# Performance work log

Measured on AMD Instinct MI355X. Metric: run time of the kernel, lower is better.

Reference implementation:

```python
import jax, jax.numpy as jnp
import numpy as np

B, L, S = 8192, 1024, 3
OUTSIDE, TM_HELIX, INSIDE = 0, 1, 2


def setup_inputs() -> dict:
    key = jax.random.key(0)
    k1, k2 = jax.random.split(key)
    emissions = jax.random.normal(k1, (B, L, S), dtype=jnp.float32)
    tags = jax.random.randint(k2, (B, L), 0, S)
    mask = jnp.ones((B, L), dtype=jnp.float32)
    t = np.zeros((S, S), dtype=np.float32)
    t[OUTSIDE, INSIDE] = -5.0
    t[INSIDE, OUTSIDE] = -5.0
    t[OUTSIDE, TM_HELIX] = 1.0
    t[INSIDE, TM_HELIX] = 1.0
    t[TM_HELIX, OUTSIDE] = 1.0
    t[TM_HELIX, INSIDE] = 1.0
    transitions = jnp.asarray(t)
    return {"emissions": emissions, "mask": mask, "transitions": transitions, "tags": tags}


def _score_sentence(emissions, tags, mask, transitions):
    # emission score of the gold tag at every position: (B, L)
    em_score = jnp.take_along_axis(emissions, tags[..., None], axis=2)[..., 0]
    # transition score between consecutive gold tags: (B, L-1)
    trans_score = transitions[tags[:, :-1], tags[:, 1:]]
    return em_score[:, 0] * mask[:, 0] + jnp.sum(
        (trans_score + em_score[:, 1:]) * mask[:, 1:], axis=1
    )


def _forward_alg(emissions, mask, transitions):
    def step(alpha, xs):
        em_t, m_t = xs  # (B, S), (B,)
        # scores[b, i, j] = alpha[b, i] + T[i, j] + em_t[b, j]
        scores = alpha[:, :, None] + transitions[None, :, :] + em_t[:, None, :]
        new_alpha = jax.nn.logsumexp(scores, axis=1)
        alpha = jnp.where(m_t[:, None] > 0, new_alpha, alpha)
        return alpha, None

    alpha0 = emissions[:, 0, :]
    xs = (jnp.swapaxes(emissions[:, 1:, :], 0, 1),  # (L-1, B, S)
          jnp.swapaxes(mask[:, 1:], 0, 1))          # (L-1, B)
    alpha, _ = jax.lax.scan(step, alpha0, xs)
    return jax.nn.logsumexp(alpha, axis=1)  # (B,)


def reference(emissions, mask, transitions, tags):
    logZ = _forward_alg(emissions, mask, transitions)
    gold = _score_sentence(emissions, tags, mask, transitions)
    return jnp.mean(logZ - gold)
```

## Files before the change

kernel.cpp:

```cpp
#include <hip/hip_runtime.h>


#define LOG2E 1.4426950408889634f
#define LN2   0.6931471805599453f

constexpr int B = 8192;
constexpr int L = 1024;
constexpr int SEQS_PER_BLOCK = 4;

__device__ __forceinline__ float fexp2(float x) { return __builtin_amdgcn_exp2f(x); }
__device__ __forceinline__ float flog2(float x) { return __builtin_amdgcn_logf(x); }

__device__ __forceinline__ float f4get(const float4& v, int c) {
  return c == 0 ? v.x : (c == 1 ? v.y : (c == 2 ? v.z : v.w));
}
__device__ __forceinline__ int i4get(const int4& v, int c) {
  return c == 0 ? v.x : (c == 1 ? v.y : (c == 2 ? v.z : v.w));
}

__device__ __forceinline__ float mux3(float x0, float x1, float x2, int i) {
  return (i == 0) ? x0 : ((i == 1) ? x1 : x2);
}
__device__ __forceinline__ float trmux(const float* __restrict__ T2, int p, int c) {
  const float r0 = mux3(T2[0], T2[1], T2[2], c);
  const float r1 = mux3(T2[3], T2[4], T2[5], c);
  const float r2 = mux3(T2[6], T2[7], T2[8], c);
  return mux3(r0, r1, r2, p);
}

__device__ __forceinline__ void matmul3(float* __restrict__ D,
                                        const float* __restrict__ A,
                                        const float* __restrict__ Bm) {
  #pragma unroll
  for (int i = 0; i < 3; ++i)
    #pragma unroll
    for (int j = 0; j < 3; ++j)
      D[i * 3 + j] = A[i * 3 + 0] * Bm[0 * 3 + j] +
                     A[i * 3 + 1] * Bm[1 * 3 + j] +
                     A[i * 3 + 2] * Bm[2 * 3 + j];
}

__device__ __forceinline__ void renorm3(float* __restrict__ P, float& scale) {
  float m = P[0];
  #pragma unroll
  for (int e = 1; e < 9; ++e) m = fmaxf(m, P[e]);
  int ex;
  (void)frexpf(m, &ex);
  #pragma unroll
  for (int e = 0; e < 9; ++e) P[e] = ldexpf(P[e], -ex);
  scale += (float)ex;
}

__global__ __launch_bounds__(256, 4) void crf_main(
    const float* __restrict__ em, const float* __restrict__ mask,
    const float* __restrict__ trans, const int* __restrict__ tags,
    float* __restrict__ out) {
  const int lane = threadIdx.x & 63;
  const int wid = threadIdx.x >> 6;
  const int b = blockIdx.x * SEQS_PER_BLOCK + wid;

  const float4* em4 = (const float4*)(em + (size_t)b * (L * 3)) + lane * 12;
  const float4* mk4 = (const float4*)(mask + (size_t)b * L) + lane * 4;
  const int4*   tg4 = (const int4*)(tags + (size_t)b * L) + lane * 4;

  float4 E[12];
  #pragma unroll
  for (int u = 0; u < 12; ++u) E[u] = em4[u];
  float4 MK[4];
  #pragma unroll
  for (int u = 0; u < 4; ++u) MK[u] = mk4[u];
  int4 TG[4];
  #pragma unroll
  for (int u = 0; u < 4; ++u) TG[u] = tg4[u];

  float T2[9], tk[9];
  #pragma unroll
  for (int e = 0; e < 9; ++e) {
    T2[e] = trans[e] * LOG2E;
    tk[e] = fexp2(T2[e]);
  }

  float P[9] = {1.f, 0.f, 0.f, 0.f, 1.f, 0.f, 0.f, 0.f, 1.f};
  float scale = 0.f, gold = 0.f;
  float a0 = 0.f, a1 = 0.f, a2 = 0.f;
  float e0_sel = 0.f, mk0 = 0.f;
  int tag0 = 0, prev = 0;

  #pragma unroll
  for (int s = 0; s < 16; ++s) {
    const float ev0 = f4get(E[(3 * s + 0) >> 2], (3 * s + 0) & 3) * LOG2E;
    const float ev1 = f4get(E[(3 * s + 1) >> 2], (3 * s + 1) & 3) * LOG2E;
    const float ev2 = f4get(E[(3 * s + 2) >> 2], (3 * s + 2) & 3) * LOG2E;
    const float m   = f4get(MK[s >> 2], s & 3);
    const int   cur = i4get(TG[s >> 2], s & 3);

    const float e = mux3(ev0, ev1, ev2, cur);
    if (s == 0) {
      e0_sel = e; mk0 = m; tag0 = cur;
    } else {
      gold = fmaf(trmux(T2, prev, cur) + e, m, gold);
    }
    prev = cur;

    const float w0 = fexp2(ev0);
    const float w1 = fexp2(ev1);
    const float w2 = fexp2(ev2);
    if (s == 0) { a0 = w0; a1 = w1; a2 = w2; }
    const bool act = (m > 0.f) && !(s == 0 && lane == 0);
    const float g  = act ? 1.f : 0.f;
    const float c1 = 1.f - g;
    const float u0 = w0 * g, u1 = w1 * g, u2 = w2 * g;
    float M[9];
    M[0] = fmaf(tk[0], u0, c1); M[1] = tk[1] * u1;           M[2] = tk[2] * u2;
    M[3] = tk[3] * u0;          M[4] = fmaf(tk[4], u1, c1);  M[5] = tk[5] * u2;
    M[6] = tk[6] * u0;          M[7] = tk[7] * u1;           M[8] = fmaf(tk[8], u2, c1);
    float N[9];
    matmul3(N, P, M);
    #pragma unroll
    for (int e2 = 0; e2 < 9; ++e2) P[e2] = N[e2];

    if (s == 7 || s == 15) renorm3(P, scale);
  }

  const int prevLast = __shfl_up(prev, 1);
  if (lane == 0) gold = fmaf(e0_sel, mk0, gold);
  else           gold = fmaf(trmux(T2, prevLast, tag0) + e0_sel, mk0, gold);
  #pragma unroll
  for (int d = 1; d < 64; d <<= 1) gold += __shfl_xor(gold, d, 64);

  #pragma unroll
  for (int d = 1; d < 64; d <<= 1) {
    float o[9];
    #pragma unroll
    for (int e = 0; e < 9; ++e) o[e] = __shfl_xor(P[e], d, 64);
    const float osc = __shfl_xor(scale, d, 64);
    const bool later = (lane & d) != 0;
    float A[9], Bm[9];
    #pragma unroll
    for (int e = 0; e < 9; ++e) {
      A[e]  = later ? o[e] : P[e];
      Bm[e] = later ? P[e] : o[e];
    }
    float N[9];
    matmul3(N, A, Bm);
    #pragma unroll
    for (int e = 0; e < 9; ++e) P[e] = N[e];
    scale += osc;
  }

  __shared__ float red[SEQS_PER_BLOCK];
  if (lane == 0) {
    const float z = a0 * (P[0] + P[1] + P[2]) +
                    a1 * (P[3] + P[4] + P[5]) +
                    a2 * (P[6] + P[7] + P[8]);
    red[wid] = LN2 * (scale + flog2(z) - gold);
  }
  __syncthreads();
  if (threadIdx.x == 0) {
    const float s = red[0] + red[1] + red[2] + red[3];
    atomicAdd(out, s * (1.0f / (float)B));
  }
}

extern "C" void kernel_launch(void* const* d_in, const int* in_sizes, int n_in,
                              void* d_out, int out_size, void* d_ws, size_t ws_size,
                              hipStream_t stream) {
  const float* em    = (const float*)d_in[0];
  const float* mask  = (const float*)d_in[1];
  const float* trans = (const float*)d_in[2];
  const int*   tags  = (const int*)d_in[3];
  float* out = (float*)d_out;

  hipMemsetAsync(out, 0, sizeof(float), stream);
  crf_main<<<B / SEQS_PER_BLOCK, 256, 0, stream>>>(em, mask, trans, tags, out);
}
```

Before: 196.3 us.

## Stage sequence halves through padded LDS with coalesced loads and prefetch

Global loads change from per-lane strided float4 chunks to fully coalesced wave-wide float4 loads. The data is transposed through padded shared memory so each lane still handles a contiguous segment of 8 steps. Each sequence is split into two halves of 512 steps: the second half is prefetched into registers while the first is computed, then the two 3x3 products are combined. This adds LDS traffic, an extra wave scan, and block-wide syncs, in exchange for better DRAM coalescing and overlap of loads with compute.

```diff
diff --git a/kernel.cpp b/kernel.cpp
--- a/kernel.cpp
+++ b/kernel.cpp
@@ -5,21 +5,16 @@
 #define LN2   0.6931471805599453f
 
 constexpr int B = 8192;
-constexpr int L = 1024;
-constexpr int SEQS_PER_BLOCK = 4;
+constexpr int W = 4;
+constexpr int EM_DW = 64 * 25;
+constexpr int MK_DW = 64 * 9;
+constexpr int TG_DW = 128;
 
 __device__ __forceinline__ float fexp2(float x) { return __builtin_amdgcn_exp2f(x); }
 __device__ __forceinline__ float flog2(float x) { return __builtin_amdgcn_logf(x); }
 
-__device__ __forceinline__ float f4get(const float4& v, int c) {
-  return c == 0 ? v.x : (c == 1 ? v.y : (c == 2 ? v.z : v.w));
-}
-__device__ __forceinline__ int i4get(const int4& v, int c) {
-  return c == 0 ? v.x : (c == 1 ? v.y : (c == 2 ? v.z : v.w));
-}
-
-__device__ __forceinline__ float mux3(float x0, float x1, float x2, int i) {
-  return (i == 0) ? x0 : ((i == 1) ? x1 : x2);
+__device__ __forceinline__ float mux3(float a, float b, float c, int i) {
+  return i == 0 ? a : (i == 1 ? b : c);
 }
 __device__ __forceinline__ float trmux(const float* __restrict__ T2, int p, int c) {
   const float r0 = mux3(T2[0], T2[1], T2[2], c);
@@ -51,82 +46,94 @@
   scale += (float)ex;
 }
 
-__global__ __launch_bounds__(256, 4) void crf_main(
-    const float* __restrict__ em, const float* __restrict__ mask,
-    const float* __restrict__ trans, const int* __restrict__ tags,
-    float* __restrict__ out) {
-  const int lane = threadIdx.x & 63;
-  const int wid = threadIdx.x >> 6;
-  const int b = blockIdx.x * SEQS_PER_BLOCK + wid;
-
-  const float4* em4 = (const float4*)(em + (size_t)b * (L * 3)) + lane * 12;
-  const float4* mk4 = (const float4*)(mask + (size_t)b * L) + lane * 4;
-  const int4*   tg4 = (const int4*)(tags + (size_t)b * L) + lane * 4;
-
-  float4 E[12];
-  #pragma unroll
-  for (int u = 0; u < 12; ++u) E[u] = em4[u];
-  float4 MK[4];
-  #pragma unroll
-  for (int u = 0; u < 4; ++u) MK[u] = mk4[u];
-  int4 TG[4];
-  #pragma unroll
-  for (int u = 0; u < 4; ++u) TG[u] = tg4[u];
-
-  float T2[9], tk[9];
-  #pragma unroll
-  for (int e = 0; e < 9; ++e) {
-    T2[e] = trans[e] * LOG2E;
-    tk[e] = fexp2(T2[e]);
-  }
-
-  float P[9] = {1.f, 0.f, 0.f, 0.f, 1.f, 0.f, 0.f, 0.f, 1.f};
-  float scale = 0.f, gold = 0.f;
-  float a0 = 0.f, a1 = 0.f, a2 = 0.f;
-  float e0_sel = 0.f, mk0 = 0.f;
+__device__ __forceinline__ void stage(float* __restrict__ E, float* __restrict__ Mk,
+                                      unsigned* __restrict__ Tg, int lane,
+                                      const float4* __restrict__ vem,
+                                      const float4* __restrict__ vmk,
+                                      const int4* __restrict__ vtg) {
+  #pragma unroll
+  for (int u = 0; u < 6; ++u) {
+    const int p = u * 64 + lane;
+    const int a = 4 * p + (int)((unsigned)p / 6u);
+    const float4 v = vem[u];
+    E[a + 0] = v.x; E[a + 1] = v.y; E[a + 2] = v.z; E[a + 3] = v.w;
+  }
+  #pragma unroll
+  for (int u = 0; u < 2; ++u) {
+    const int p = u * 64 + lane;
+    const int a = 4 * p + (p >> 1);
+    const float4 v = vmk[u];
+    Mk[a + 0] = v.x; Mk[a + 1] = v.y; Mk[a + 2] = v.z; Mk[a + 3] = v.w;
+  }
+  #pragma unroll
+  for (int u = 0; u < 2; ++u) {
+    const int p = u * 64 + lane;
+    const int4 t = vtg[u];
+    Tg[p] = (unsigned)(t.x & 3) | ((unsigned)(t.y & 3) << 8) |
+            ((unsigned)(t.z & 3) << 16) | ((unsigned)(t.w & 3) << 24);
+  }
+}
+
+template <bool FIRST>
+__device__ __forceinline__ void compute_round(
+    const float* __restrict__ E, const float* __restrict__ Mk,
+    const unsigned* __restrict__ Tg, int lane,
+    const float* __restrict__ T2, const float* __restrict__ tk,
+    float* __restrict__ Pout, float& scaleOut,
+    float& gold, int& lastTag, int boundaryTag, float* __restrict__ a012) {
+  const float* eml = E + 25 * lane;
+  const float* mkl = Mk + 9 * lane;
+  const unsigned t0 = Tg[2 * lane + 0];
+  const unsigned t1 = Tg[2 * lane + 1];
+
+  float P[9];
+  float scale = 0.f;
+  float e0sel = 0.f, mk0 = 0.f;
   int tag0 = 0, prev = 0;
 
   #pragma unroll
-  for (int s = 0; s < 16; ++s) {
-    const float ev0 = f4get(E[(3 * s + 0) >> 2], (3 * s + 0) & 3) * LOG2E;
-    const float ev1 = f4get(E[(3 * s + 1) >> 2], (3 * s + 1) & 3) * LOG2E;
-    const float ev2 = f4get(E[(3 * s + 2) >> 2], (3 * s + 2) & 3) * LOG2E;
-    const float m   = f4get(MK[s >> 2], s & 3);
-    const int   cur = i4get(TG[s >> 2], s & 3);
+  for (int j = 0; j < 8; ++j) {
+    const float ev0 = eml[3 * j + 0] * LOG2E;
+    const float ev1 = eml[3 * j + 1] * LOG2E;
+    const float ev2 = eml[3 * j + 2] * LOG2E;
+    const float m = mkl[j];
+    const unsigned tw = (j < 4) ? t0 : t1;
+    const int cur = (int)((tw >> (8 * (j & 3))) & 3u);
 
     const float e = mux3(ev0, ev1, ev2, cur);
-    if (s == 0) {
-      e0_sel = e; mk0 = m; tag0 = cur;
-    } else {
-      gold = fmaf(trmux(T2, prev, cur) + e, m, gold);
-    }
+    if (j == 0) { e0sel = e; mk0 = m; tag0 = cur; }
+    else        gold = fmaf(trmux(T2, prev, cur) + e, m, gold);
     prev = cur;
 
     const float w0 = fexp2(ev0);
     const float w1 = fexp2(ev1);
     const float w2 = fexp2(ev2);
-    if (s == 0) { a0 = w0; a1 = w1; a2 = w2; }
-    const bool act = (m > 0.f) && !(s == 0 && lane == 0);
-    const float g  = act ? 1.f : 0.f;
+    if (FIRST && j == 0) { a012[0] = w0; a012[1] = w1; a012[2] = w2; }
+    const bool act = (m > 0.f) && !(FIRST && j == 0 && lane == 0);
+    const float g = act ? 1.f : 0.f;
     const float c1 = 1.f - g;
     const float u0 = w0 * g, u1 = w1 * g, u2 = w2 * g;
     float M[9];
-    M[0] = fmaf(tk[0], u0, c1); M[1] = tk[1] * u1;           M[2] = tk[2] * u2;
-    M[3] = tk[3] * u0;          M[4] = fmaf(tk[4], u1, c1);  M[5] = tk[5] * u2;
-    M[6] = tk[6] * u0;          M[7] = tk[7] * u1;           M[8] = fmaf(tk[8], u2, c1);
-    float N[9];
-    matmul3(N, P, M);
-    #pragma unroll
-    for (int e2 = 0; e2 < 9; ++e2) P[e2] = N[e2];
-
-    if (s == 7 || s == 15) renorm3(P, scale);
-  }
-
-  const int prevLast = __shfl_up(prev, 1);
-  if (lane == 0) gold = fmaf(e0_sel, mk0, gold);
-  else           gold = fmaf(trmux(T2, prevLast, tag0) + e0_sel, mk0, gold);
-  #pragma unroll
-  for (int d = 1; d < 64; d <<= 1) gold += __shfl_xor(gold, d, 64);
+    M[0] = fmaf(tk[0], u0, c1); M[1] = tk[1] * u1;          M[2] = tk[2] * u2;
+    M[3] = tk[3] * u0;          M[4] = fmaf(tk[4], u1, c1); M[5] = tk[5] * u2;
+    M[6] = tk[6] * u0;          M[7] = tk[7] * u1;          M[8] = fmaf(tk[8], u2, c1);
+    if (j == 0) {
+      #pragma unroll
+      for (int e2 = 0; e2 < 9; ++e2) P[e2] = M[e2];
+    } else {
+      float N[9];
+      matmul3(N, P, M);
+      #pragma unroll
+      for (int e2 = 0; e2 < 9; ++e2) P[e2] = N[e2];
+    }
+  }
+  renorm3(P, scale);
+
+  const int prevLast = __shfl_up(prev, 1, 64);
+  const int bt = (lane == 0) ? boundaryTag : prevLast;
+  if (FIRST && lane == 0) gold = fmaf(e0sel, mk0, gold);
+  else                    gold = fmaf(trmux(T2, bt, tag0) + e0sel, mk0, gold);
+  lastTag = prev;
 
   #pragma unroll
   for (int d = 1; d < 64; d <<= 1) {
@@ -147,13 +154,80 @@
     for (int e = 0; e < 9; ++e) P[e] = N[e];
     scale += osc;
   }
-
-  __shared__ float red[SEQS_PER_BLOCK];
+  #pragma unroll
+  for (int e = 0; e < 9; ++e) Pout[e] = P[e];
+  scaleOut = scale;
+}
+
+__global__ __launch_bounds__(256, 4) void crf_main(
+    const float* __restrict__ em, const float* __restrict__ mask,
+    const float* __restrict__ trans, const int* __restrict__ tags,
+    float* __restrict__ out) {
+  __shared__ float s_em[W][EM_DW];
+  __shared__ float s_mk[W][MK_DW];
+  __shared__ unsigned s_tg[W][TG_DW];
+  __shared__ float red[W];
+
+  const int lane = threadIdx.x & 63;
+  const int wid = threadIdx.x >> 6;
+  const int b = blockIdx.x * W + wid;
+
+  const float4* em4 = (const float4*)(em + (size_t)b * 3072);
+  const float4* mk4 = (const float4*)(mask + (size_t)b * 1024);
+  const int4*   tg4 = (const int4*)(tags + (size_t)b * 1024);
+
+  float4 aem[6], amk[2]; int4 atg[2];
+  #pragma unroll
+  for (int u = 0; u < 6; ++u) aem[u] = em4[u * 64 + lane];
+  #pragma unroll
+  for (int u = 0; u < 2; ++u) amk[u] = mk4[u * 64 + lane];
+  #pragma unroll
+  for (int u = 0; u < 2; ++u) atg[u] = tg4[u * 64 + lane];
+
+  float T2[9], tk[9];
+  #pragma unroll
+  for (int e = 0; e < 9; ++e) {
+    T2[e] = trans[e] * LOG2E;
+    tk[e] = fexp2(T2[e]);
+  }
+
+  stage(s_em[wid], s_mk[wid], s_tg[wid], lane, aem, amk, atg);
+  __syncthreads();
+
+  float4 pem[6], pmk[2]; int4 ptg[2];
+  #pragma unroll
+  for (int u = 0; u < 6; ++u) pem[u] = em4[384 + u * 64 + lane];
+  #pragma unroll
+  for (int u = 0; u < 2; ++u) pmk[u] = mk4[128 + u * 64 + lane];
+  #pragma unroll
+  for (int u = 0; u < 2; ++u) ptg[u] = tg4[128 + u * 64 + lane];
+
+  float gold = 0.f;
+  float a012[3];
+  float PA[9], PB[9];
+  float scA, scB;
+  int lastA, lastB;
+
+  compute_round<true>(s_em[wid], s_mk[wid], s_tg[wid], lane, T2, tk,
+                      PA, scA, gold, lastA, 0, a012);
+
+  stage(s_em[wid], s_mk[wid], s_tg[wid], lane, pem, pmk, ptg);
+  __syncthreads();
+
+  const int tag511 = __shfl(lastA, 63, 64);
+  compute_round<false>(s_em[wid], s_mk[wid], s_tg[wid], lane, T2, tk,
+                       PB, scB, gold, lastB, tag511, a012);
+
+  #pragma unroll
+  for (int d = 1; d < 64; d <<= 1) gold += __shfl_xor(gold, d, 64);
+
   if (lane == 0) {
-    const float z = a0 * (P[0] + P[1] + P[2]) +
-                    a1 * (P[3] + P[4] + P[5]) +
-                    a2 * (P[6] + P[7] + P[8]);
-    red[wid] = LN2 * (scale + flog2(z) - gold);
+    float P[9];
+    matmul3(P, PA, PB);
+    const float z = a012[0] * (P[0] + P[1] + P[2]) +
+                    a012[1] * (P[3] + P[4] + P[5]) +
+                    a012[2] * (P[6] + P[7] + P[8]);
+    red[wid] = LN2 * (scA + scB + flog2(z) - gold);
   }
   __syncthreads();
   if (threadIdx.x == 0) {
@@ -172,5 +246,5 @@
   float* out = (float*)d_out;
 
   hipMemsetAsync(out, 0, sizeof(float), stream);
-  crf_main<<<B / SEQS_PER_BLOCK, 256, 0, stream>>>(em, mask, trans, tags, out);
-}
+  crf_main<<<B / W, 256, 0, stream>>>(em, mask, trans, tags, out);
+}
```

Result: slower. 275.0 us (+40.1%).

## Coalesce emission loads via LDS transpose and process sequence in four chunks

Applied to the files above, without the earlier changes.

Instead of each lane loading 48 contiguous floats (strided across lanes), the wavefront now loads coalesced float4 rows and transposes emissions through padded LDS, processing the sequence in four 256-step chunks with double-buffered register prefetch. Each chunk does a per-lane 4-step matrix product, a wave-wide shuffle scan, and accumulates into a running product, with gold-score boundary tags carried across chunks. This is meant to fix uncoalesced global access and cut register pressure, at the cost of four shuffle reductions instead of one plus extra LDS traffic.

```diff
diff --git a/kernel.cpp b/kernel.cpp
--- a/kernel.cpp
+++ b/kernel.cpp
@@ -5,21 +5,14 @@
 #define LN2   0.6931471805599453f
 
 constexpr int B = 8192;
-constexpr int L = 1024;
-constexpr int SEQS_PER_BLOCK = 4;
+constexpr int W = 4;
+constexpr int LSTRIDE = 14;
 
 __device__ __forceinline__ float fexp2(float x) { return __builtin_amdgcn_exp2f(x); }
 __device__ __forceinline__ float flog2(float x) { return __builtin_amdgcn_logf(x); }
 
-__device__ __forceinline__ float f4get(const float4& v, int c) {
-  return c == 0 ? v.x : (c == 1 ? v.y : (c == 2 ? v.z : v.w));
-}
-__device__ __forceinline__ int i4get(const int4& v, int c) {
-  return c == 0 ? v.x : (c == 1 ? v.y : (c == 2 ? v.z : v.w));
-}
-
-__device__ __forceinline__ float mux3(float x0, float x1, float x2, int i) {
-  return (i == 0) ? x0 : ((i == 1) ? x1 : x2);
+__device__ __forceinline__ float mux3(float a, float b, float c, int i) {
+  return i == 0 ? a : (i == 1 ? b : c);
 }
 __device__ __forceinline__ float trmux(const float* __restrict__ T2, int p, int c) {
   const float r0 = mux3(T2[0], T2[1], T2[2], c);
@@ -55,104 +48,159 @@
     const float* __restrict__ em, const float* __restrict__ mask,
     const float* __restrict__ trans, const int* __restrict__ tags,
     float* __restrict__ out) {
+  __shared__ __align__(16) float s_em[W][64 * LSTRIDE];
+  __shared__ float red[W];
+
   const int lane = threadIdx.x & 63;
-  const int wid = threadIdx.x >> 6;
-  const int b = blockIdx.x * SEQS_PER_BLOCK + wid;
-
-  const float4* em4 = (const float4*)(em + (size_t)b * (L * 3)) + lane * 12;
-  const float4* mk4 = (const float4*)(mask + (size_t)b * L) + lane * 4;
-  const int4*   tg4 = (const int4*)(tags + (size_t)b * L) + lane * 4;
-
-  float4 E[12];
-  #pragma unroll
-  for (int u = 0; u < 12; ++u) E[u] = em4[u];
-  float4 MK[4];
-  #pragma unroll
-  for (int u = 0; u < 4; ++u) MK[u] = mk4[u];
-  int4 TG[4];
-  #pragma unroll
-  for (int u = 0; u < 4; ++u) TG[u] = tg4[u];
+  const int wid  = threadIdx.x >> 6;
+  const int b    = blockIdx.x * W + wid;
+  float* lds = s_em[wid];
+
+  const float4* em4 = (const float4*)(em + (size_t)b * 3072);
+  const float4* mk4 = (const float4*)(mask + (size_t)b * 1024);
+  const int4*   tg4 = (const int4*)(tags + (size_t)b * 1024);
+
+  float4 em_r[2][3]; float4 mk_r[2]; int4 tg_r[2];
+  #pragma unroll
+  for (int u = 0; u < 3; ++u) em_r[0][u] = em4[u * 64 + lane];
+  mk_r[0] = mk4[lane];
+  tg_r[0] = tg4[lane];
+  #pragma unroll
+  for (int u = 0; u < 3; ++u) em_r[1][u] = em4[192 + u * 64 + lane];
+  mk_r[1] = mk4[64 + lane];
+  tg_r[1] = tg4[64 + lane];
 
   float T2[9], tk[9];
   #pragma unroll
-  for (int e = 0; e < 9; ++e) {
-    T2[e] = trans[e] * LOG2E;
-    tk[e] = fexp2(T2[e]);
-  }
-
-  float P[9] = {1.f, 0.f, 0.f, 0.f, 1.f, 0.f, 0.f, 0.f, 1.f};
+  for (int e = 0; e < 9; ++e) { T2[e] = trans[e] * LOG2E; tk[e] = fexp2(T2[e]); }
+
+  float Pacc[9];
   float scale = 0.f, gold = 0.f;
   float a0 = 0.f, a1 = 0.f, a2 = 0.f;
-  float e0_sel = 0.f, mk0 = 0.f;
-  int tag0 = 0, prev = 0;
-
-  #pragma unroll
-  for (int s = 0; s < 16; ++s) {
-    const float ev0 = f4get(E[(3 * s + 0) >> 2], (3 * s + 0) & 3) * LOG2E;
-    const float ev1 = f4get(E[(3 * s + 1) >> 2], (3 * s + 1) & 3) * LOG2E;
-    const float ev2 = f4get(E[(3 * s + 2) >> 2], (3 * s + 2) & 3) * LOG2E;
-    const float m   = f4get(MK[s >> 2], s & 3);
-    const int   cur = i4get(TG[s >> 2], s & 3);
-
-    const float e = mux3(ev0, ev1, ev2, cur);
-    if (s == 0) {
-      e0_sel = e; mk0 = m; tag0 = cur;
+  int boundaryTag = 0;
+
+  #pragma unroll
+  for (int q = 0; q < 4; ++q) {
+    const int buf = q & 1;
+
+    #pragma unroll
+    for (int u = 0; u < 3; ++u) {
+      const float4 v = em_r[buf][u];
+      const int t  = u + lane;
+      const int l0 = 21 * u + t / 3;
+      const int r0 = 4 * (t % 3);
+      float2* wp = (float2*)&lds[l0 * LSTRIDE + r0];
+      wp[0] = make_float2(v.x, v.y);
+      wp[1] = make_float2(v.z, v.w);
+    }
+
+    const float mf[4] = {mk_r[buf].x, mk_r[buf].y, mk_r[buf].z, mk_r[buf].w};
+    const int   tf[4] = {tg_r[buf].x, tg_r[buf].y, tg_r[buf].z, tg_r[buf].w};
+
+    float P[9];
+    float e0sel = 0.f, mk0 = 0.f;
+    int tag0 = 0, prev = 0;
+    const float2* rp = (const float2*)&lds[lane * LSTRIDE];
+
+    #pragma unroll
+    for (int h = 0; h < 2; ++h) {
+      float eb[6];
+      #pragma unroll
+      for (int r = 0; r < 3; ++r) {
+        const float2 t = rp[3 * h + r];
+        eb[2 * r] = t.x; eb[2 * r + 1] = t.y;
+      }
+      #pragma unroll
+      for (int jj = 0; jj < 2; ++jj) {
+        const int j = 2 * h + jj;
+        const float ev0 = eb[3 * jj + 0] * LOG2E;
+        const float ev1 = eb[3 * jj + 1] * LOG2E;
+        const float ev2 = eb[3 * jj + 2] * LOG2E;
+        const float m = mf[j];
+        const int cur = tf[j];
+
+        const float e = mux3(ev0, ev1, ev2, cur);
+        if (j == 0) { e0sel = e; mk0 = m; tag0 = cur; }
+        else        gold = fmaf(trmux(T2, prev, cur) + e, m, gold);
+        prev = cur;
+
+        const float w0 = fexp2(ev0), w1 = fexp2(ev1), w2 = fexp2(ev2);
+        if (q == 0 && j == 0) { a0 = w0; a1 = w1; a2 = w2; }
+        const bool act = (m > 0.f) && !(q == 0 && j == 0 && lane == 0);
+        const float g = act ? 1.f : 0.f;
+        const float c1 = 1.f - g;
+        const float u0 = w0 * g, u1 = w1 * g, u2 = w2 * g;
+        float M[9];
+        M[0] = fmaf(tk[0], u0, c1); M[1] = tk[1] * u1;          M[2] = tk[2] * u2;
+        M[3] = tk[3] * u0;          M[4] = fmaf(tk[4], u1, c1); M[5] = tk[5] * u2;
+        M[6] = tk[6] * u0;          M[7] = tk[7] * u1;          M[8] = fmaf(tk[8], u2, c1);
+        if (j == 0) {
+          #pragma unroll
+          for (int e2 = 0; e2 < 9; ++e2) P[e2] = M[e2];
+        } else {
+          float N[9];
+          matmul3(N, P, M);
+          #pragma unroll
+          for (int e2 = 0; e2 < 9; ++e2) P[e2] = N[e2];
+        }
+      }
+    }
+
+    const int prevLast = __shfl_up(prev, 1, 64);
+    const int bt = (lane == 0) ? boundaryTag : prevLast;
+    const float tr0 = trmux(T2, bt, tag0);
+    const float tplus = (q == 0 && lane == 0) ? 0.f : tr0;
+    gold = fmaf(tplus + e0sel, mk0, gold);
+    boundaryTag = __shfl(prev, 63, 64);
+
+    float sc = 0.f;
+    renorm3(P, sc);
+    #pragma unroll
+    for (int d = 1; d < 64; d <<= 1) {
+      float o[9];
+      #pragma unroll
+      for (int e2 = 0; e2 < 9; ++e2) o[e2] = __shfl_xor(P[e2], d, 64);
+      const float osc = __shfl_xor(sc, d, 64);
+      const bool later = (lane & d) != 0;
+      float A[9], Bm[9];
+      #pragma unroll
+      for (int e2 = 0; e2 < 9; ++e2) {
+        A[e2]  = later ? o[e2] : P[e2];
+        Bm[e2] = later ? P[e2] : o[e2];
+      }
+      float N[9];
+      matmul3(N, A, Bm);
+      #pragma unroll
+      for (int e2 = 0; e2 < 9; ++e2) P[e2] = N[e2];
+      sc += osc;
+    }
+    scale += sc;
+
+    if (q == 0) {
+      #pragma unroll
+      for (int e2 = 0; e2 < 9; ++e2) Pacc[e2] = P[e2];
     } else {
-      gold = fmaf(trmux(T2, prev, cur) + e, m, gold);
-    }
-    prev = cur;
-
-    const float w0 = fexp2(ev0);
-    const float w1 = fexp2(ev1);
-    const float w2 = fexp2(ev2);
-    if (s == 0) { a0 = w0; a1 = w1; a2 = w2; }
-    const bool act = (m > 0.f) && !(s == 0 && lane == 0);
-    const float g  = act ? 1.f : 0.f;
-    const float c1 = 1.f - g;
-    const float u0 = w0 * g, u1 = w1 * g, u2 = w2 * g;
-    float M[9];
-    M[0] = fmaf(tk[0], u0, c1); M[1] = tk[1] * u1;           M[2] = tk[2] * u2;
-    M[3] = tk[3] * u0;          M[4] = fmaf(tk[4], u1, c1);  M[5] = tk[5] * u2;
-    M[6] = tk[6] * u0;          M[7] = tk[7] * u1;           M[8] = fmaf(tk[8], u2, c1);
-    float N[9];
-    matmul3(N, P, M);
-    #pragma unroll
-    for (int e2 = 0; e2 < 9; ++e2) P[e2] = N[e2];
-
-    if (s == 7 || s == 15) renorm3(P, scale);
+      float N[9];
+      matmul3(N, Pacc, P);
+      #pragma unroll
+      for (int e2 = 0; e2 < 9; ++e2) Pacc[e2] = N[e2];
+    }
+
+    if (q < 2) {
+      #pragma unroll
+      for (int u = 0; u < 3; ++u) em_r[buf][u] = em4[(q + 2) * 192 + u * 64 + lane];
+      mk_r[buf] = mk4[(q + 2) * 64 + lane];
+      tg_r[buf] = tg4[(q + 2) * 64 + lane];
+    }
   }
 
-  const int prevLast = __shfl_up(prev, 1);
-  if (lane == 0) gold = fmaf(e0_sel, mk0, gold);
-  else           gold = fmaf(trmux(T2, prevLast, tag0) + e0_sel, mk0, gold);
   #pragma unroll
   for (int d = 1; d < 64; d <<= 1) gold += __shfl_xor(gold, d, 64);
 
-  #pragma unroll
-  for (int d = 1; d < 64; d <<= 1) {
-    float o[9];
-    #pragma unroll
-    for (int e = 0; e < 9; ++e) o[e] = __shfl_xor(P[e], d, 64);
-    const float osc = __shfl_xor(scale, d, 64);
-    const bool later = (lane & d) != 0;
-    float A[9], Bm[9];
-    #pragma unroll
-    for (int e = 0; e < 9; ++e) {
-      A[e]  = later ? o[e] : P[e];
-      Bm[e] = later ? P[e] : o[e];
-    }
-    float N[9];
-    matmul3(N, A, Bm);
-    #pragma unroll
-    for (int e = 0; e < 9; ++e) P[e] = N[e];
-    scale += osc;
-  }
-
-  __shared__ float red[SEQS_PER_BLOCK];
   if (lane == 0) {
-    const float z = a0 * (P[0] + P[1] + P[2]) +
-                    a1 * (P[3] + P[4] + P[5]) +
-                    a2 * (P[6] + P[7] + P[8]);
+    const float z = a0 * (Pacc[0] + Pacc[1] + Pacc[2]) +
+                    a1 * (Pacc[3] + Pacc[4] + Pacc[5]) +
+                    a2 * (Pacc[6] + Pacc[7] + Pacc[8]);
     red[wid] = LN2 * (scale + flog2(z) - gold);
   }
   __syncthreads();
@@ -172,5 +220,5 @@
   float* out = (float*)d_out;
 
   hipMemsetAsync(out, 0, sizeof(float), stream);
-  crf_main<<<B / SEQS_PER_BLOCK, 256, 0, stream>>>(em, mask, trans, tags, out);
-}
+  crf_main<<<B / W, 256, 0, stream>>>(em, mask, trans, tags, out);
+}
```

New measurement: 227.1 us. 15.7% more time.
